# Optimization experiments

Measured on AMD Instinct MI355X. Metric: run time of the kernel, lower is better.

The kernel has to match this reference:

```python
import jax, jax.numpy as jnp
import numpy as np

N, T, M, D, H, FD, FF, L, B = 24, 120, 3, 32, 2, 16, 64, 3, 64
SCALE = 1.0 / np.sqrt(FD)  # torch MHA scales q by 1/sqrt(head_dim)
NEG = -1e9


def _make_pe():
    # Faithful to the module's (nonstandard) encoding: denominator uses 2*i/D for every i.
    t = np.arange(T, dtype=np.float64)[:, None]
    i = np.arange(D, dtype=np.float64)[None, :]
    denom = np.power(10000.0, 2.0 * i / D)
    pe = np.where(i % 2 == 0, np.sin(t / denom), np.cos(t / denom))
    return jnp.asarray(pe, jnp.float32)  # (T, D)


def _ln(x, g, b):
    mu = x.mean(-1, keepdims=True)
    var = x.var(-1, keepdims=True)
    return (x - mu) / jnp.sqrt(var + 1e-5) * g + b


def setup_inputs() -> dict:
    key = jax.random.key(0)
    keys = iter(jax.random.split(key, 48))
    def nrm(shape, s=0.1):
        return jax.random.normal(next(keys), shape, jnp.float32) * s
    inp = {
        'X': jax.random.normal(next(keys), (B, T, N * M), jnp.float32),
        'pe': _make_pe(),
        'E_W': nrm((N, M, D)), 'E_b': nrm((N, D), 0.01),
        'tq_W': nrm((N, D, D)), 'tq_b': nrm((N, D), 0.01),
        'tk_W': nrm((N, D, D)), 'tk_b': nrm((N, D), 0.01),
        'tv_W': nrm((N, D, D)), 'tv_b': nrm((N, D), 0.01),
        'tm_Wq': nrm((N, D, D)), 'tm_bq': nrm((N, D), 0.01),
        'tm_Wk': nrm((N, D, D)), 'tm_bk': nrm((N, D), 0.01),
        'tm_Wv': nrm((N, D, D)), 'tm_bv': nrm((N, D), 0.01),
        'tm_Wo': nrm((N, D, D)), 'tm_bo': nrm((N, D), 0.01),
        'sq_W': nrm((T, D, D)), 'sq_b': nrm((T, D), 0.01),
        'sk_W': nrm((T, D, D)), 'sk_b': nrm((T, D), 0.01),
        'sv_W': nrm((T, D, D)), 'sv_b': nrm((T, D), 0.01),
        'sm_Wq': nrm((T, D, D)), 'sm_bq': nrm((T, D), 0.01),
        'sm_Wk': nrm((T, D, D)), 'sm_bk': nrm((T, D), 0.01),
        'sm_Wv': nrm((T, D, D)), 'sm_bv': nrm((T, D), 0.01),
        'sm_Wo': nrm((T, D, D)), 'sm_bo': nrm((T, D), 0.01),
        'ff1_W': nrm((D, FF)), 'ff1_b': nrm((FF,), 0.01),
        'ff2_W': nrm((FF, D)), 'ff2_b': nrm((D,), 0.01),
        'ln_g': jnp.ones((D,), jnp.float32), 'ln_b': jnp.zeros((D,), jnp.float32),
        'op_W': nrm((N, D, M)), 'op_b': nrm((N, M), 0.01),
    }
    return inp


def reference(X, pe, E_W, E_b, tq_W, tq_b, tk_W, tk_b, tv_W, tv_b,
              tm_Wq, tm_bq, tm_Wk, tm_bk, tm_Wv, tm_bv, tm_Wo, tm_bo,
              sq_W, sq_b, sk_W, sk_b, sv_W, sv_b,
              sm_Wq, sm_bq, sm_Wk, sm_bk, sm_Wv, sm_bv, sm_Wo, sm_bo,
              ff1_W, ff1_b, ff2_W, ff2_b, ln_g, ln_b, op_W, op_b):
    b = X.shape[0]
    Xr = X.reshape(b, T, N, M)
    # per-joint embedding + positional encoding (dropout = identity in eval)
    E = jnp.einsum('btnm,nmd->btnd', Xr, E_W) + E_b + pe[None, :, None, :]
    causal = jnp.triu(jnp.full((T, T), NEG, jnp.float32), 1)
    for _ in range(L):
        # ---- temporal attention: per node n, causal over time ----
        q = jnp.einsum('btnd,nde->btne', E, tq_W) + tq_b
        k = jnp.einsum('btnd,nde->btne', E, tk_W) + tk_b
        v = jnp.einsum('btnd,nde->btne', E, tv_W) + tv_b
        qp = (jnp.einsum('btnd,nde->btne', q, tm_Wq) + tm_bq).reshape(b, T, N, H, FD)
        kp = (jnp.einsum('btnd,nde->btne', k, tm_Wk) + tm_bk).reshape(b, T, N, H, FD)
        vp = (jnp.einsum('btnd,nde->btne', v, tm_Wv) + tm_bv).reshape(b, T, N, H, FD)
        scores = jnp.einsum('bqnhf,bknhf->bnhqk', qp, kp) * SCALE + causal
        attn = jax.nn.softmax(scores, axis=-1)
        o = jnp.einsum('bnhqk,bknhf->bqnhf', attn, vp).reshape(b, T, N, D)
        t_sum = jnp.einsum('btnd,nde->btne', o, tm_Wo) + tm_bo
        t_norm = _ln(E + t_sum, ln_g, ln_b)
        # ---- spatial attention: per timestep t, full over nodes ----
        q = jnp.einsum('btnd,tde->btne', E, sq_W) + sq_b[:, None]
        k = jnp.einsum('btnd,tde->btne', E, sk_W) + sk_b[:, None]
        v = jnp.einsum('btnd,tde->btne', E, sv_W) + sv_b[:, None]
        qp = (jnp.einsum('btnd,tde->btne', q, sm_Wq) + sm_bq[:, None]).reshape(b, T, N, H, FD)
        kp = (jnp.einsum('btnd,tde->btne', k, sm_Wk) + sm_bk[:, None]).reshape(b, T, N, H, FD)
        vp = (jnp.einsum('btnd,tde->btne', v, sm_Wv) + sm_bv[:, None]).reshape(b, T, N, H, FD)
        scores = jnp.einsum('btqhf,btkhf->bthqk', qp, kp) * SCALE
        attn = jax.nn.softmax(scores, axis=-1)
        o = jnp.einsum('bthqk,btkhf->btqhf', attn, vp).reshape(b, T, N, D)
        s_sum = jnp.einsum('btnd,tde->btne', o, sm_Wo) + sm_bo[:, None]
        s_norm = _ln(E + s_sum, ln_g, ln_b)
        # ---- shared feedforward + norm ----
        ts = t_norm + s_norm
        ff = jax.nn.relu(ts @ ff1_W + ff1_b) @ ff2_W + ff2_b
        E = _ln(ff + ts, ln_g, ln_b)
    out = jnp.einsum('btnd,ndm->btnm', E, op_W) + op_b
    return out.reshape(b, T, N * M) + X
```

## Files before the change

### kernel.cpp

```cpp
#include <hip/hip_runtime.h>
#include <hip/hip_bf16.h>

typedef __hip_bfloat16 bf16;
typedef __fp16 h2 __attribute__((ext_vector_type(2)));
typedef _Float16 f16x2 __attribute__((ext_vector_type(2)));

constexpr int B  = 64, T = 120, N = 24, M = 3, D = 32;
constexpr int NH = 2, FD = 16, FF = 64, L = 3;
constexpr float SCALE = 0.25f;
constexpr int SK  = 40;
constexpr int SOH = 20;
constexpr int CH2 = 30;
constexpr int NJ  = 30;
constexpr int QR  = 64;
constexpr int QCH = (B * T) / QR;
constexpr int QEH = 20;
constexpr int BG  = 2;
constexpr int SR  = N * BG;
constexpr int SEH = 20;
constexpr int FR  = 32;
constexpr int QG  = N * QCH;
constexpr int SG  = T * (B / BG);

__device__ __forceinline__ float b2f(bf16 x) { return __bfloat162float(x); }
__device__ __forceinline__ float blo(unsigned u) { return __uint_as_float(u << 16); }
__device__ __forceinline__ float bhi(unsigned u) { return __uint_as_float(u & 0xffff0000u); }
__device__ __forceinline__ unsigned pk2(float a, float b) {
  bf16 x = __float2bfloat16(a), y = __float2bfloat16(b);
  unsigned short ux = *reinterpret_cast<unsigned short*>(&x);
  unsigned short uy = *reinterpret_cast<unsigned short*>(&y);
  return (unsigned)ux | ((unsigned)uy << 16);
}
__device__ __forceinline__ unsigned pkh2(float a, float b) {
  h2 r = __builtin_amdgcn_cvt_pkrtz(a, b);
  return *reinterpret_cast<unsigned*>(&r);
}
__device__ __forceinline__ h2 u2h(unsigned u) { return *reinterpret_cast<h2*>(&u); }
__device__ __forceinline__ f16x2 u2f(unsigned u) { return *reinterpret_cast<f16x2*>(&u); }

__global__ __launch_bounds__(256) void compose3_kernel(
    const float* __restrict__ W1q, const float* __restrict__ b1q,
    const float* __restrict__ W2q, const float* __restrict__ b2q,
    const float* __restrict__ W1k, const float* __restrict__ b1k,
    const float* __restrict__ W2k, const float* __restrict__ b2k,
    const float* __restrict__ W1v, const float* __restrict__ b1v,
    const float* __restrict__ W2v, const float* __restrict__ b2v,
    float* __restrict__ Wc, float* __restrict__ bc, int U) {
  int fam = blockIdx.x / U;
  int n   = blockIdx.x % U;
  const float* W1 = (fam == 0) ? W1q : (fam == 1) ? W1k : W1v;
  const float* b1 = (fam == 0) ? b1q : (fam == 1) ? b1k : b1v;
  const float* W2 = (fam == 0) ? W2q : (fam == 1) ? W2k : W2v;
  const float* b2 = (fam == 0) ? b2q : (fam == 1) ? b2k : b2v;
  const float* w1 = W1 + n * D * D;
  const float* w2 = W2 + n * D * D;
  float* wc  = Wc + (size_t)(fam * U + n) * D * D;
  float* bcp = bc + (fam * U + n) * D;
  __shared__ float s1[D * D], s2[D * D];
  for (int i = threadIdx.x; i < D * D; i += 256) { s1[i] = w1[i]; s2[i] = w2[i]; }
  __syncthreads();
  for (int i = threadIdx.x; i < D * D; i += 256) {
    int d = i >> 5, f = i & 31;
    float acc = 0.f;
#pragma unroll
    for (int e = 0; e < D; ++e) acc += s1[d * D + e] * s2[e * D + f];
    wc[i] = acc;
  }
  if (threadIdx.x < D) {
    int f = threadIdx.x;
    float acc = b2[n * D + f];
#pragma unroll
    for (int e = 0; e < D; ++e) acc += b1[n * D + e] * s2[e * D + f];
    bcp[f] = acc;
  }
}

__global__ __launch_bounds__(256) void embed_kernel(
    const float* __restrict__ X, const float* __restrict__ pe,
    const float* __restrict__ E_W, const float* __restrict__ E_b,
    bf16* __restrict__ E) {
  int idx = blockIdx.x * 256 + threadIdx.x;
  if (idx >= B * T * N * D) return;
  int d = idx & 31;
  int n = (idx >> 5) % N;
  int bt = idx / (D * N);
  int t = bt % T;
  const float* x = X + bt * (N * M) + n * M;
  float acc = E_b[n * D + d] + pe[t * D + d];
#pragma unroll
  for (int m = 0; m < M; ++m) acc += x[m] * E_W[(n * M + m) * D + d];
  E[idx] = __float2bfloat16(acc);
}

struct QSmem {
  unsigned whh[3 * (D / 2) * D];
  float bsh[3 * D];
  unsigned Esp[QR * QEH];
};
struct SSmem {
  unsigned Wh[3 * (D / 2) * D];
  unsigned woh[(D / 2) * D];
  float bqs[D], bks[D], bvs[D], bos[D], gs[D], bbs[D];
  unsigned Esh[SR * SEH];
  __fp16 Qh[SR * SK];
  __fp16 Kh[SR * SK];
  __fp16 Vh[SR * SK];
};
constexpr size_t FUSED_SMEM =
    sizeof(SSmem) > sizeof(QSmem) ? sizeof(SSmem) : sizeof(QSmem);

__global__ __launch_bounds__(256) void qs_fused_kernel(
    const bf16* __restrict__ E, const float* __restrict__ WtC,
    const float* __restrict__ btC,
    bf16* __restrict__ Qt, bf16* __restrict__ Kt, bf16* __restrict__ Vt,
    const float* __restrict__ WsC, const float* __restrict__ bsC,
    const float* __restrict__ sm_Wo, const float* __restrict__ sm_bo,
    const float* __restrict__ ln_g, const float* __restrict__ ln_b,
    bf16* __restrict__ Sn, int qblocks) {
  __shared__ __align__(16) char smem[FUSED_SMEM];
  int tid = threadIdx.x;

  if ((int)blockIdx.x < qblocks) {
    QSmem& q = *reinterpret_cast<QSmem*>(smem);
    int n     = blockIdx.x / QCH;
    int chunk = blockIdx.x % QCH;
    for (int i = tid; i < 3 * (D / 2) * D; i += 256) {
      int fam = i / ((D / 2) * D);
      int idx = i % ((D / 2) * D);
      int d2 = idx >> 5, j = idx & 31;
      const float* wg = WtC + (size_t)(fam * N + n) * D * D;
      q.whh[i] = pkh2(wg[(2 * d2) * D + j], wg[(2 * d2 + 1) * D + j]);
    }
    if (tid < 3 * D) {
      int fam = tid >> 5, e = tid & 31;
      q.bsh[tid] = btC[(fam * N + n) * D + e];
    }
    {
      int row = tid >> 2, p = tid & 3;
      const bf16* er = E + ((size_t)(chunk * QR + row) * N + n) * D;
      uint4 u = *(const uint4*)&er[p * 8];
      uint4 o;
      o.x = pkh2(blo(u.x), bhi(u.x));
      o.y = pkh2(blo(u.y), bhi(u.y));
      o.z = pkh2(blo(u.z), bhi(u.z));
      o.w = pkh2(blo(u.w), bhi(u.w));
      *(uint4*)&q.Esp[row * QEH + p * 4] = o;
    }
    __syncthreads();

    int row = tid >> 2, qd = tid & 3;
    int grow = chunk * QR + row;
    int b = grow / T, t = grow % T;
    unsigned xp[D / 2];
#pragma unroll
    for (int d2 = 0; d2 < D / 2; ++d2) xp[d2] = q.Esp[row * QEH + d2];
    size_t dsto = (((size_t)b * N + n) * T + t) * D + qd * 8;
    bf16* dsts[3] = { Qt + dsto, Kt + dsto, Vt + dsto };
#pragma unroll
    for (int fam = 0; fam < 3; ++fam) {
      const unsigned* wf = q.whh + fam * (D / 2) * D;
      const float* bi = q.bsh + fam * D;
      float a[8];
#pragma unroll
      for (int j = 0; j < 8; ++j) a[j] = bi[qd * 8 + j];
#pragma unroll
      for (int d2 = 0; d2 < D / 2; ++d2) {
        h2 x = u2h(xp[d2]);
#pragma unroll
        for (int j = 0; j < 8; ++j)
          a[j] = __builtin_amdgcn_fdot2(x, u2h(wf[d2 * D + qd * 8 + j]), a[j], false);
      }
      uint4 o;
      o.x = pk2(a[0], a[1]); o.y = pk2(a[2], a[3]);
      o.z = pk2(a[4], a[5]); o.w = pk2(a[6], a[7]);
      *(uint4*)dsts[fam] = o;
    }
  } else {
    SSmem& s = *reinterpret_cast<SSmem*>(smem);
    int sb = blockIdx.x - qblocks;
    int t  = sb >> 5;
    int bg = sb & 31;
    int b0 = bg * BG;

    for (int i = tid; i < 3 * (D / 2) * D; i += 256) {
      int fam = i / ((D / 2) * D);
      int idx = i % ((D / 2) * D);
      int d2 = idx >> 5, e = idx & 31;
      const float* wg = WsC + (size_t)(fam * T + t) * D * D;
      s.Wh[i] = pkh2(wg[(2 * d2) * D + e], wg[(2 * d2 + 1) * D + e]);
    }
    {
      const float* wg = sm_Wo + (size_t)t * D * D;
      for (int i = tid; i < (D / 2) * D; i += 256) {
        int d2 = i >> 5, e = i & 31;
        s.woh[i] = pkh2(wg[(2 * d2) * D + e], wg[(2 * d2 + 1) * D + e]);
      }
    }
    if (tid < D) {
      s.bqs[tid] = bsC[(0 * T + t) * D + tid];
      s.bks[tid] = bsC[(1 * T + t) * D + tid];
      s.bvs[tid] = bsC[(2 * T + t) * D + tid];
      s.bos[tid] = sm_bo[t * D + tid];
      s.gs[tid]  = ln_g[tid];
      s.bbs[tid] = ln_b[tid];
    }
    if (tid < SR * 4) {
      int r = tid >> 2, p = tid & 3;
      int b = b0 + r / N, n = r % N;
      uint4 u = *(const uint4*)&E[(((size_t)b * T + t) * N + n) * D + p * 8];
      uint4 o;
      o.x = pkh2(blo(u.x), bhi(u.x));
      o.y = pkh2(blo(u.y), bhi(u.y));
      o.z = pkh2(blo(u.z), bhi(u.z));
      o.w = pkh2(blo(u.w), bhi(u.w));
      *(uint4*)&s.Esh[r * SEH + p * 4] = o;
    }
    __syncthreads();

#pragma unroll 1
    for (int i = tid; i < SR * D; i += 256) {
      int r = i >> 5, e = i & 31;
      float aq = s.bqs[e], ak = s.bks[e], av = s.bvs[e];
#pragma unroll
      for (int d2 = 0; d2 < D / 2; ++d2) {
        h2 x = u2h(s.Esh[r * SEH + d2]);
        aq = __builtin_amdgcn_fdot2(x, u2h(s.Wh[0 * 512 + d2 * 32 + e]), aq, false);
        ak = __builtin_amdgcn_fdot2(x, u2h(s.Wh[1 * 512 + d2 * 32 + e]), ak, false);
        av = __builtin_amdgcn_fdot2(x, u2h(s.Wh[2 * 512 + d2 * 32 + e]), av, false);
      }
      s.Qh[r * SK + e] = (__fp16)aq;
      s.Kh[r * SK + e] = (__fp16)ak;
      s.Vh[r * SK + e] = (__fp16)av;
    }
    __syncthreads();

    if (tid < SR * NH) {
      int r = tid >> 1, h = tid & 1, ho = h * FD;
      int kb = (r >= N) ? N : 0;
      uint4 q0 = *(const uint4*)&s.Qh[r * SK + ho];
      uint4 q1 = *(const uint4*)&s.Qh[r * SK + ho + 8];
      unsigned qh[8] = { q0.x, q0.y, q0.z, q0.w, q1.x, q1.y, q1.z, q1.w };
      float sc[N];
      float m = -1e30f;
#pragma unroll
      for (int k = 0; k < N; ++k) {
        const uint4 ka = *(const uint4*)&s.Kh[(kb + k) * SK + ho];
        const uint4 kc = *(const uint4*)&s.Kh[(kb + k) * SK + ho + 8];
        float s0 = __builtin_amdgcn_fdot2(u2h(qh[0]), u2h(ka.x), 0.f, false);
        float s1 = __builtin_amdgcn_fdot2(u2h(qh[1]), u2h(ka.y), 0.f, false);
        float s2 = __builtin_amdgcn_fdot2(u2h(qh[2]), u2h(ka.z), 0.f, false);
        float s3 = __builtin_amdgcn_fdot2(u2h(qh[3]), u2h(ka.w), 0.f, false);
        s0 = __builtin_amdgcn_fdot2(u2h(qh[4]), u2h(kc.x), s0, false);
        s1 = __builtin_amdgcn_fdot2(u2h(qh[5]), u2h(kc.y), s1, false);
        s2 = __builtin_amdgcn_fdot2(u2h(qh[6]), u2h(kc.z), s2, false);
        s3 = __builtin_amdgcn_fdot2(u2h(qh[7]), u2h(kc.w), s3, false);
        float sv = ((s0 + s1) + (s2 + s3)) * SCALE;
        sc[k] = sv;
        m = fmaxf(m, sv);
      }
      float l = 0.f;
#pragma unroll
      for (int k = 0; k < N; ++k) { sc[k] = __expf(sc[k] - m); l += sc[k]; }
      float rl = 1.f / l;

      f16x2 acc2[8];
#pragma unroll
      for (int f = 0; f < 8; ++f) acc2[f] = f16x2{(_Float16)0.f, (_Float16)0.f};
#pragma unroll
      for (int k = 0; k < N; ++k) {
        f16x2 pp = f16x2{(_Float16)sc[k], (_Float16)sc[k]};
        const uint4 va = *(const uint4*)&s.Vh[(kb + k) * SK + ho];
        const uint4 vb = *(const uint4*)&s.Vh[(kb + k) * SK + ho + 8];
        acc2[0] += pp * u2f(va.x);
        acc2[1] += pp * u2f(va.y);
        acc2[2] += pp * u2f(va.z);
        acc2[3] += pp * u2f(va.w);
        acc2[4] += pp * u2f(vb.x);
        acc2[5] += pp * u2f(vb.y);
        acc2[6] += pp * u2f(vb.z);
        acc2[7] += pp * u2f(vb.w);
      }
      unsigned* op = (unsigned*)&s.Qh[r * SK + ho];
#pragma unroll
      for (int j = 0; j < 8; ++j)
        op[j] = pkh2((float)acc2[j][0] * rl, (float)acc2[j][1] * rl);
    }
    __syncthreads();

#pragma unroll 1
    for (int it = 0; it < 2; ++it) {
      int rl = it * 32 + (tid >> 3);
      int qd = tid & 7, e0 = qd * 4;
      if (rl < SR) {
        const unsigned* opk = (const unsigned*)&s.Qh[rl * SK];
        unsigned r0u = s.Esh[rl * SEH + (e0 >> 1)];
        unsigned r1u = s.Esh[rl * SEH + (e0 >> 1) + 1];
        h2 ra = u2h(r0u), rb = u2h(r1u);
        float res[4] = { (float)ra[0], (float)ra[1], (float)rb[0], (float)rb[1] };
        float o[4], s1 = 0.f, s2 = 0.f;
#pragma unroll
        for (int j = 0; j < 4; ++j) {
          int e = e0 + j;
          float a = s.bos[e] + res[j];
#pragma unroll
          for (int d2 = 0; d2 < D / 2; ++d2)
            a = __builtin_amdgcn_fdot2(u2h(opk[d2]), u2h(s.woh[d2 * D + e]), a, false);
          o[j] = a; s1 += a; s2 += a * a;
        }
        s1 += __shfl_xor(s1, 1, 64); s2 += __shfl_xor(s2, 1, 64);
        s1 += __shfl_xor(s1, 2, 64); s2 += __shfl_xor(s2, 2, 64);
        s1 += __shfl_xor(s1, 4, 64); s2 += __shfl_xor(s2, 4, 64);
        float mu  = s1 * (1.f / D);
        float var = s2 * (1.f / D) - mu * mu;
        float rr = rsqrtf(var + 1e-5f);
        int b = b0 + rl / N, n = rl % N;
        uint2 ou;
        ou.x = pk2((o[0]-mu)*rr*s.gs[e0]+s.bbs[e0],    (o[1]-mu)*rr*s.gs[e0+1]+s.bbs[e0+1]);
        ou.y = pk2((o[2]-mu)*rr*s.gs[e0+2]+s.bbs[e0+2],(o[3]-mu)*rr*s.gs[e0+3]+s.bbs[e0+3]);
        *(uint2*)&Sn[(((size_t)b * T + t) * N + n) * D + e0] = ou;
      }
    }
  }
}

__global__ __launch_bounds__(256) void attnt_kernel(
    const bf16* __restrict__ Qt, const bf16* __restrict__ Kt,
    const bf16* __restrict__ Vt, const bf16* __restrict__ E,
    const float* __restrict__ tm_Wo, const float* __restrict__ tm_bo,
    const float* __restrict__ ln_g, const float* __restrict__ ln_b,
    bf16* __restrict__ Tn) {
  int bn = blockIdx.x;
  int n  = bn % N, b = bn / N;
  __shared__ __align__(16) __fp16 Klh[T * SK];
  __shared__ __align__(16) __fp16 Vlh[T * SK];
  __shared__ __align__(16) __fp16 Qlh[CH2 * SK];
  __shared__ __align__(16) unsigned Olh[CH2 * SOH];
  __shared__ unsigned woh[(D / 2) * D];
  __shared__ float bol[D], gl[D], bbl[D];
  int tid = threadIdx.x;

  const bf16* Kg = Kt + (size_t)bn * T * D;
  const bf16* Vg = Vt + (size_t)bn * T * D;
  const bf16* Qg = Qt + (size_t)bn * T * D;
  for (int i = tid; i < T * 4; i += 256) {
    int r = i >> 2, p = i & 3;
    uint4 ku = *(const uint4*)&Kg[r * D + p * 8];
    uint4 kh;
    kh.x = pkh2(blo(ku.x), bhi(ku.x));
    kh.y = pkh2(blo(ku.y), bhi(ku.y));
    kh.z = pkh2(blo(ku.z), bhi(ku.z));
    kh.w = pkh2(blo(ku.w), bhi(ku.w));
    *(uint4*)&Klh[r * SK + p * 8] = kh;
    uint4 vu = *(const uint4*)&Vg[r * D + p * 8];
    uint4 vh;
    vh.x = pkh2(blo(vu.x), bhi(vu.x));
    vh.y = pkh2(blo(vu.y), bhi(vu.y));
    vh.z = pkh2(blo(vu.z), bhi(vu.z));
    vh.w = pkh2(blo(vu.w), bhi(vu.w));
    *(uint4*)&Vlh[r * SK + p * 8] = vh;
  }
  {
    const float* wg = tm_Wo + (size_t)n * D * D;
    for (int i = tid; i < (D / 2) * D; i += 256) {
      int d2 = i >> 5, e = i & 31;
      woh[i] = pkh2(wg[(2 * d2) * D + e], wg[(2 * d2 + 1) * D + e]);
    }
  }
  if (tid < D) {
    bol[tid] = tm_bo[n * D + tid];
    gl[tid]  = ln_g[tid];
    bbl[tid] = ln_b[tid];
  }
  __syncthreads();

#pragma unroll
  for (int c = 0; c < 4; ++c) {
    const int JM = (CH2 * (c + 1) + 3) >> 2;
    if (tid < CH2 * 4) {
      int r = tid >> 2, p = tid & 3;
      uint4 qu = *(const uint4*)&Qg[(CH2 * c + r) * D + p * 8];
      uint4 qh;
      qh.x = pkh2(blo(qu.x), bhi(qu.x));
      qh.y = pkh2(blo(qu.y), bhi(qu.y));
      qh.z = pkh2(blo(qu.z), bhi(qu.z));
      qh.w = pkh2(blo(qu.w), bhi(qu.w));
      *(uint4*)&Qlh[r * SK + p * 8] = qh;
    }
    __syncthreads();

    {
      int task = tid >> 2, sl = tid & 3;
      if (task < 2 * CH2) {
        int rl = task >> 1, h = task & 1, ho = h * FD;
        int rg = CH2 * c + rl;
        uint4 q0 = *(const uint4*)&Qlh[rl * SK + ho];
        uint4 q1 = *(const uint4*)&Qlh[rl * SK + ho + 8];
        unsigned qh[8] = { q0.x, q0.y, q0.z, q0.w, q1.x, q1.y, q1.z, q1.w };

        float sc[NJ];
        float mx = -3e38f;
#pragma unroll
        for (int j = 0; j < JM; ++j) {
          int k = 4 * j + sl;
          sc[j] = -3e38f;
          if (k <= rg) {
            const uint4 ka = *(const uint4*)&Klh[k * SK + ho];
            const uint4 kb = *(const uint4*)&Klh[k * SK + ho + 8];
            float s0 = __builtin_amdgcn_fdot2(u2h(qh[0]), u2h(ka.x), 0.f, false);
            float s1 = __builtin_amdgcn_fdot2(u2h(qh[1]), u2h(ka.y), 0.f, false);
            float s2 = __builtin_amdgcn_fdot2(u2h(qh[2]), u2h(ka.z), 0.f, false);
            float s3 = __builtin_amdgcn_fdot2(u2h(qh[3]), u2h(ka.w), 0.f, false);
            s0 = __builtin_amdgcn_fdot2(u2h(qh[4]), u2h(kb.x), s0, false);
            s1 = __builtin_amdgcn_fdot2(u2h(qh[5]), u2h(kb.y), s1, false);
            s2 = __builtin_amdgcn_fdot2(u2h(qh[6]), u2h(kb.z), s2, false);
            s3 = __builtin_amdgcn_fdot2(u2h(qh[7]), u2h(kb.w), s3, false);
            float s = ((s0 + s1) + (s2 + s3)) * SCALE;
            sc[j] = s;
            mx = fmaxf(mx, s);
          }
        }
        mx = fmaxf(mx, __shfl_xor(mx, 1, 64));
        mx = fmaxf(mx, __shfl_xor(mx, 2, 64));
        float l = 0.f;
#pragma unroll
        for (int j = 0; j < JM; ++j) {
          sc[j] = __expf(sc[j] - mx);
          l += sc[j];
        }
        l += __shfl_xor(l, 1, 64);
        l += __shfl_xor(l, 2, 64);
        float rli = 1.f / l;

        f16x2 acc2[8];
#pragma unroll
        for (int f = 0; f < 8; ++f) acc2[f] = f16x2{(_Float16)0.f, (_Float16)0.f};
#pragma unroll
        for (int j = 0; j < JM; ++j) {
          int k = 4 * j + sl;
          if (k <= rg) {
            f16x2 pp = f16x2{(_Float16)sc[j], (_Float16)sc[j]};
            const uint4 va = *(const uint4*)&Vlh[k * SK + ho];
            const uint4 vb = *(const uint4*)&Vlh[k * SK + ho + 8];
            acc2[0] += pp * u2f(va.x);
            acc2[1] += pp * u2f(va.y);
            acc2[2] += pp * u2f(va.z);
            acc2[3] += pp * u2f(va.w);
            acc2[4] += pp * u2f(vb.x);
            acc2[5] += pp * u2f(vb.y);
            acc2[6] += pp * u2f(vb.z);
            acc2[7] += pp * u2f(vb.w);
          }
        }
#pragma unroll
        for (int f = 0; f < 8; ++f) {
          unsigned u = *reinterpret_cast<unsigned*>(&acc2[f]);
          unsigned u1 = __shfl_xor(u, 1, 64);
          acc2[f] += u2f(u1);
          u = *reinterpret_cast<unsigned*>(&acc2[f]);
          unsigned u2_ = __shfl_xor(u, 2, 64);
          acc2[f] += u2f(u2_);
        }
        if (sl == 0) {
#pragma unroll
          for (int j = 0; j < 8; ++j)
            Olh[rl * SOH + h * 8 + j] =
                pkh2((float)acc2[j][0] * rli, (float)acc2[j][1] * rli);
        }
      }
    }
    __syncthreads();

    {
      int rl = tid >> 3, q = tid & 7, e0 = q * 4;
      if (rl < CH2) {
        int rg = CH2 * c + rl;
        size_t rowo = ((size_t)(b * T + rg) * N + n) * D;
        uint2 eu = *(const uint2*)&E[rowo + e0];
        float res[4] = { blo(eu.x), bhi(eu.x), blo(eu.y), bhi(eu.y) };
        float o[4], s1 = 0.f, s2 = 0.f;
#pragma unroll
        for (int j = 0; j < 4; ++j) {
          int e = e0 + j;
          float a = bol[e] + res[j];
#pragma unroll
          for (int d2 = 0; d2 < D / 2; ++d2)
            a = __builtin_amdgcn_fdot2(u2h(Olh[rl * SOH + d2]),
                                       u2h(woh[d2 * D + e]), a, false);
          o[j] = a; s1 += a; s2 += a * a;
        }
        s1 += __shfl_xor(s1, 1, 64); s2 += __shfl_xor(s2, 1, 64);
        s1 += __shfl_xor(s1, 2, 64); s2 += __shfl_xor(s2, 2, 64);
        s1 += __shfl_xor(s1, 4, 64); s2 += __shfl_xor(s2, 4, 64);
        float mu  = s1 * (1.f / D);
        float var = s2 * (1.f / D) - mu * mu;
        float r = rsqrtf(var + 1e-5f);
        uint2 ou;
        ou.x = pk2((o[0]-mu)*r*gl[e0]+bbl[e0],    (o[1]-mu)*r*gl[e0+1]+bbl[e0+1]);
        ou.y = pk2((o[2]-mu)*r*gl[e0+2]+bbl[e0+2],(o[3]-mu)*r*gl[e0+3]+bbl[e0+3]);
        *(uint2*)&Tn[rowo + e0] = ou;
      }
    }
  }
}

__global__ __launch_bounds__(256) void ff_kernel(
    const bf16* __restrict__ Tn, const bf16* __restrict__ Sn,
    const float* __restrict__ W1, const float* __restrict__ b1,
    const float* __restrict__ W2, const float* __restrict__ b2,
    const float* __restrict__ ln_g, const float* __restrict__ ln_b,
    bf16* __restrict__ E) {
  __shared__ unsigned w1h[(D / 2) * FF];
  __shared__ unsigned w2h[(FF / 2) * D];
  __shared__ float bb1[FF], bb2[D], gs[D], bbs[D];
  __shared__ unsigned tslp[FR][D / 2 + 1];
  __shared__ unsigned hlp[FR][FF / 2 + 1];
  int tid = threadIdx.x;
  int r0 = blockIdx.x * FR;
  for (int i = tid; i < (D / 2) * FF; i += 256) {
    int d2 = i / FF, jj = i % FF;
    w1h[i] = pkh2(W1[(2 * d2) * FF + jj], W1[(2 * d2 + 1) * FF + jj]);
  }
  for (int i = tid; i < (FF / 2) * D; i += 256) {
    int k2 = i / D, e = i % D;
    w2h[i] = pkh2(W2[(2 * k2) * D + e], W2[(2 * k2 + 1) * D + e]);
  }
  if (tid < FF) bb1[tid] = b1[tid];
  if (tid < D) { bb2[tid] = b2[tid]; gs[tid] = ln_g[tid]; bbs[tid] = ln_b[tid]; }
  int r = tid >> 3, s = tid & 7;
  {
    const bf16* tp = Tn + ((size_t)(r0 + r)) * D + s * 4;
    const bf16* sp = Sn + ((size_t)(r0 + r)) * D + s * 4;
    uint2 tu = *(const uint2*)tp;
    uint2 su = *(const uint2*)sp;
    float t0 = blo(tu.x) + blo(su.x);
    float t1 = bhi(tu.x) + bhi(su.x);
    float t2 = blo(tu.y) + blo(su.y);
    float t3 = bhi(tu.y) + bhi(su.y);
    tslp[r][s * 2]     = pkh2(t0, t1);
    tslp[r][s * 2 + 1] = pkh2(t2, t3);
  }
  __syncthreads();
  {
    float hh[8];
#pragma unroll
    for (int j = 0; j < 8; ++j) {
      int jj = s * 8 + j;
      float a = bb1[jj];
#pragma unroll
      for (int d2 = 0; d2 < D / 2; ++d2)
        a = __builtin_amdgcn_fdot2(u2h(tslp[r][d2]), u2h(w1h[d2 * FF + jj]), a, false);
      hh[j] = fmaxf(a, 0.f);
    }
#pragma unroll
    for (int j = 0; j < 4; ++j)
      hlp[r][s * 4 + j] = pkh2(hh[2 * j], hh[2 * j + 1]);
  }
  __syncthreads();
  {
    float x[4];
    float s1 = 0.f, s2 = 0.f;
#pragma unroll
    for (int j4 = 0; j4 < 4; ++j4) {
      int e = s * 4 + j4;
      h2 tv = u2h(tslp[r][e >> 1]);
      float a = bb2[e] + (float)tv[j4 & 1];
#pragma unroll
      for (int k2 = 0; k2 < FF / 2; ++k2)
        a = __builtin_amdgcn_fdot2(u2h(hlp[r][k2]), u2h(w2h[k2 * D + e]), a, false);
      x[j4] = a; s1 += a; s2 += a * a;
    }
    s1 += __shfl_xor(s1, 1, 64); s2 += __shfl_xor(s2, 1, 64);
    s1 += __shfl_xor(s1, 2, 64); s2 += __shfl_xor(s2, 2, 64);
    s1 += __shfl_xor(s1, 4, 64); s2 += __shfl_xor(s2, 4, 64);
    float mu  = s1 * (1.f / D);
    float var = s2 * (1.f / D) - mu * mu;
    float rr = rsqrtf(var + 1e-5f);
    int e0 = s * 4;
    uint2 ou;
    ou.x = pk2((x[0]-mu)*rr*gs[e0]+bbs[e0],    (x[1]-mu)*rr*gs[e0+1]+bbs[e0+1]);
    ou.y = pk2((x[2]-mu)*rr*gs[e0+2]+bbs[e0+2],(x[3]-mu)*rr*gs[e0+3]+bbs[e0+3]);
    *(uint2*)&E[((size_t)(r0 + r)) * D + e0] = ou;
  }
}

__global__ __launch_bounds__(256) void out_kernel(
    const bf16* __restrict__ E, const float* __restrict__ op_W,
    const float* __restrict__ op_b, const float* __restrict__ X,
    float* __restrict__ out) {
  int idx = blockIdx.x * 256 + threadIdx.x;
  if (idx >= B * T * N * M) return;
  int m  = idx % M;
  int n  = (idx / M) % N;
  int bt = idx / (M * N);
  float acc = op_b[n * M + m];
  const bf16* e = E + ((size_t)bt * N + n) * D;
#pragma unroll
  for (int d = 0; d < D; ++d) acc += b2f(e[d]) * op_W[(n * D + d) * M + m];
  acc += X[idx];
  out[idx] = acc;
}

extern "C" void kernel_launch(void* const* d_in, const int* in_sizes, int n_in,
                              void* d_out, int out_size, void* d_ws, size_t ws_size,
                              hipStream_t stream) {
  const float* X     = (const float*)d_in[0];
  const float* pe    = (const float*)d_in[1];
  const float* E_W   = (const float*)d_in[2];
  const float* E_b   = (const float*)d_in[3];
  const float* tq_W  = (const float*)d_in[4];
  const float* tq_b  = (const float*)d_in[5];
  const float* tk_W  = (const float*)d_in[6];
  const float* tk_b  = (const float*)d_in[7];
  const float* tv_W  = (const float*)d_in[8];
  const float* tv_b  = (const float*)d_in[9];
  const float* tm_Wq = (const float*)d_in[10];
  const float* tm_bq = (const float*)d_in[11];
  const float* tm_Wk = (const float*)d_in[12];
  const float* tm_bk = (const float*)d_in[13];
  const float* tm_Wv = (const float*)d_in[14];
  const float* tm_bv = (const float*)d_in[15];
  const float* tm_Wo = (const float*)d_in[16];
  const float* tm_bo = (const float*)d_in[17];
  const float* sq_W  = (const float*)d_in[18];
  const float* sq_b  = (const float*)d_in[19];
  const float* sk_W  = (const float*)d_in[20];
  const float* sk_b  = (const float*)d_in[21];
  const float* sv_W  = (const float*)d_in[22];
  const float* sv_b  = (const float*)d_in[23];
  const float* sm_Wq = (const float*)d_in[24];
  const float* sm_bq = (const float*)d_in[25];
  const float* sm_Wk = (const float*)d_in[26];
  const float* sm_bk = (const float*)d_in[27];
  const float* sm_Wv = (const float*)d_in[28];
  const float* sm_bv = (const float*)d_in[29];
  const float* sm_Wo = (const float*)d_in[30];
  const float* sm_bo = (const float*)d_in[31];
  const float* ff1_W = (const float*)d_in[32];
  const float* ff1_b = (const float*)d_in[33];
  const float* ff2_W = (const float*)d_in[34];
  const float* ff2_b = (const float*)d_in[35];
  const float* ln_g  = (const float*)d_in[36];
  const float* ln_b  = (const float*)d_in[37];
  const float* op_W  = (const float*)d_in[38];
  const float* op_b  = (const float*)d_in[39];
  float* out = (float*)d_out;

  float* WtC = (float*)d_ws;
  float* btC = WtC + 3 * N * D * D;
  float* WsC = btC + 3 * N * D;
  float* bsC = WsC + 3 * T * D * D;
  size_t act = (size_t)B * T * N * D;
  bf16* Ebuf = (bf16*)(bsC + 3 * T * D);
  bf16* Tn   = Ebuf + act;
  bf16* Qt   = Tn + act;
  bf16* Kt   = Qt + act;
  bf16* Vt   = Kt + act;

  size_t floats_bytes = (size_t)(3 * N * D * D + 3 * N * D +
                                 3 * T * D * D + 3 * T * D) * sizeof(float);
  size_t need6 = floats_bytes + 6 * act * sizeof(bf16);
  bool concurrent = (ws_size >= need6);
  bf16* Sn = concurrent ? (Vt + act) : Qt;

  compose3_kernel<<<3 * N, 256, 0, stream>>>(
      tq_W, tq_b, tm_Wq, tm_bq, tk_W, tk_b, tm_Wk, tm_bk,
      tv_W, tv_b, tm_Wv, tm_bv, WtC, btC, N);
  compose3_kernel<<<3 * T, 256, 0, stream>>>(
      sq_W, sq_b, sm_Wq, sm_bq, sk_W, sk_b, sm_Wk, sm_bk,
      sv_W, sv_b, sm_Wv, sm_bv, WsC, bsC, T);

  embed_kernel<<<(B * T * N * D) / 256, 256, 0, stream>>>(X, pe, E_W, E_b, Ebuf);

  for (int l = 0; l < L; ++l) {
    if (concurrent) {
      qs_fused_kernel<<<QG + SG, 256, 0, stream>>>(
          Ebuf, WtC, btC, Qt, Kt, Vt,
          WsC, bsC, sm_Wo, sm_bo, ln_g, ln_b, Sn, QG);
      attnt_kernel<<<B * N, 256, 0, stream>>>(Qt, Kt, Vt, Ebuf, tm_Wo, tm_bo, ln_g, ln_b, Tn);
    } else {
      qs_fused_kernel<<<QG, 256, 0, stream>>>(
          Ebuf, WtC, btC, Qt, Kt, Vt,
          WsC, bsC, sm_Wo, sm_bo, ln_g, ln_b, Sn, QG);
      attnt_kernel<<<B * N, 256, 0, stream>>>(Qt, Kt, Vt, Ebuf, tm_Wo, tm_bo, ln_g, ln_b, Tn);
      qs_fused_kernel<<<SG, 256, 0, stream>>>(
          Ebuf, WtC, btC, Qt, Kt, Vt,
          WsC, bsC, sm_Wo, sm_bo, ln_g, ln_b, Sn, 0);
    }
    ff_kernel<<<(B * T * N) / FR, 256, 0, stream>>>(Tn, Sn, ff1_W, ff1_b, ff2_W, ff2_b, ln_g, ln_b, Ebuf);
  }

  out_kernel<<<(B * T * N * M + 255) / 256, 256, 0, stream>>>(Ebuf, op_W, op_b, X, out);
}
```

Baseline: 422.8 us.

## Co-schedule temporal attention with spatial attention instead of with QKV projection

Splits the temporal QKV projection into its own kernel and fuses temporal attention with the spatial-attention branch in one launch, selected by block index. The spatial branch previously overlapped the cheap QKV projection and temporal attention ran alone afterwards. Now the two heavy attention phases share one grid. The launch count per layer stays the same, but the shared-memory union gets larger, which may reduce occupancy.

```diff
diff --git a/kernel.cpp b/kernel.cpp
--- a/kernel.cpp
+++ b/kernel.cpp
@@ -20,6 +20,7 @@
 constexpr int SEH = 20;
 constexpr int FR  = 32;
 constexpr int QG  = N * QCH;
+constexpr int AG  = B * N;
 constexpr int SG  = T * (B / BG);
 
 __device__ __forceinline__ float b2f(bf16 x) { return __bfloat162float(x); }
@@ -92,12 +93,78 @@
   E[idx] = __float2bfloat16(acc);
 }
 
-struct QSmem {
-  unsigned whh[3 * (D / 2) * D];
-  float bsh[3 * D];
-  unsigned Esp[QR * QEH];
+__global__ __launch_bounds__(256) void qkvt_kernel(
+    const bf16* __restrict__ E, const float* __restrict__ WtC,
+    const float* __restrict__ btC,
+    bf16* __restrict__ Qt, bf16* __restrict__ Kt, bf16* __restrict__ Vt) {
+  int n     = blockIdx.x / QCH;
+  int chunk = blockIdx.x % QCH;
+  __shared__ unsigned whh[3 * (D / 2) * D];
+  __shared__ float bsh[3 * D];
+  __shared__ __align__(16) unsigned Esp[QR * QEH];
+  int tid = threadIdx.x;
+  for (int i = tid; i < 3 * (D / 2) * D; i += 256) {
+    int fam = i / ((D / 2) * D);
+    int idx = i % ((D / 2) * D);
+    int d2 = idx >> 5, j = idx & 31;
+    const float* wg = WtC + (size_t)(fam * N + n) * D * D;
+    whh[i] = pkh2(wg[(2 * d2) * D + j], wg[(2 * d2 + 1) * D + j]);
+  }
+  if (tid < 3 * D) {
+    int fam = tid >> 5, e = tid & 31;
+    bsh[tid] = btC[(fam * N + n) * D + e];
+  }
+  {
+    int row = tid >> 2, p = tid & 3;
+    const bf16* er = E + ((size_t)(chunk * QR + row) * N + n) * D;
+    uint4 u = *(const uint4*)&er[p * 8];
+    uint4 o;
+    o.x = pkh2(blo(u.x), bhi(u.x));
+    o.y = pkh2(blo(u.y), bhi(u.y));
+    o.z = pkh2(blo(u.z), bhi(u.z));
+    o.w = pkh2(blo(u.w), bhi(u.w));
+    *(uint4*)&Esp[row * QEH + p * 4] = o;
+  }
+  __syncthreads();
+
+  int row = tid >> 2, q = tid & 3;
+  int grow = chunk * QR + row;
+  int b = grow / T, t = grow % T;
+  unsigned xp[D / 2];
+#pragma unroll
+  for (int d2 = 0; d2 < D / 2; ++d2) xp[d2] = Esp[row * QEH + d2];
+  size_t dsto = (((size_t)b * N + n) * T + t) * D + q * 8;
+  bf16* dsts[3] = { Qt + dsto, Kt + dsto, Vt + dsto };
+#pragma unroll
+  for (int fam = 0; fam < 3; ++fam) {
+    const unsigned* wf = whh + fam * (D / 2) * D;
+    const float* bi = bsh + fam * D;
+    float a[8];
+#pragma unroll
+    for (int j = 0; j < 8; ++j) a[j] = bi[q * 8 + j];
+#pragma unroll
+    for (int d2 = 0; d2 < D / 2; ++d2) {
+      h2 x = u2h(xp[d2]);
+#pragma unroll
+      for (int j = 0; j < 8; ++j)
+        a[j] = __builtin_amdgcn_fdot2(x, u2h(wf[d2 * D + q * 8 + j]), a[j], false);
+    }
+    uint4 o;
+    o.x = pk2(a[0], a[1]); o.y = pk2(a[2], a[3]);
+    o.z = pk2(a[4], a[5]); o.w = pk2(a[6], a[7]);
+    *(uint4*)dsts[fam] = o;
+  }
+}
+
+struct ASmemA {
+  __fp16 Klh[T * SK];
+  __fp16 Vlh[T * SK];
+  __fp16 Qlh[CH2 * SK];
+  unsigned Olh[CH2 * SOH];
+  unsigned woh[(D / 2) * D];
+  float bol[D], gl[D], bbl[D];
 };
-struct SSmem {
+struct ASmemS {
   unsigned Wh[3 * (D / 2) * D];
   unsigned woh[(D / 2) * D];
   float bqs[D], bks[D], bvs[D], bos[D], gs[D], bbs[D];
@@ -106,78 +173,190 @@
   __fp16 Kh[SR * SK];
   __fp16 Vh[SR * SK];
 };
-constexpr size_t FUSED_SMEM =
-    sizeof(SSmem) > sizeof(QSmem) ? sizeof(SSmem) : sizeof(QSmem);
-
-__global__ __launch_bounds__(256) void qs_fused_kernel(
-    const bf16* __restrict__ E, const float* __restrict__ WtC,
-    const float* __restrict__ btC,
-    bf16* __restrict__ Qt, bf16* __restrict__ Kt, bf16* __restrict__ Vt,
+constexpr size_t AS_SMEM =
+    sizeof(ASmemA) > sizeof(ASmemS) ? sizeof(ASmemA) : sizeof(ASmemS);
+
+__global__ __launch_bounds__(256) void as_fused_kernel(
+    const bf16* __restrict__ Qt, const bf16* __restrict__ Kt,
+    const bf16* __restrict__ Vt, const bf16* __restrict__ E,
+    const float* __restrict__ tm_Wo, const float* __restrict__ tm_bo,
     const float* __restrict__ WsC, const float* __restrict__ bsC,
     const float* __restrict__ sm_Wo, const float* __restrict__ sm_bo,
     const float* __restrict__ ln_g, const float* __restrict__ ln_b,
-    bf16* __restrict__ Sn, int qblocks) {
-  __shared__ __align__(16) char smem[FUSED_SMEM];
+    bf16* __restrict__ Tn, bf16* __restrict__ Sn, int ablocks) {
+  __shared__ __align__(16) char smem[AS_SMEM];
   int tid = threadIdx.x;
 
-  if ((int)blockIdx.x < qblocks) {
-    QSmem& q = *reinterpret_cast<QSmem*>(smem);
-    int n     = blockIdx.x / QCH;
-    int chunk = blockIdx.x % QCH;
-    for (int i = tid; i < 3 * (D / 2) * D; i += 256) {
-      int fam = i / ((D / 2) * D);
-      int idx = i % ((D / 2) * D);
-      int d2 = idx >> 5, j = idx & 31;
-      const float* wg = WtC + (size_t)(fam * N + n) * D * D;
-      q.whh[i] = pkh2(wg[(2 * d2) * D + j], wg[(2 * d2 + 1) * D + j]);
-    }
-    if (tid < 3 * D) {
-      int fam = tid >> 5, e = tid & 31;
-      q.bsh[tid] = btC[(fam * N + n) * D + e];
+  if ((int)blockIdx.x < ablocks) {
+    ASmemA& A = *reinterpret_cast<ASmemA*>(smem);
+    int bn = blockIdx.x;
+    int n  = bn % N, b = bn / N;
+
+    const bf16* Kg = Kt + (size_t)bn * T * D;
+    const bf16* Vg = Vt + (size_t)bn * T * D;
+    const bf16* Qg = Qt + (size_t)bn * T * D;
+    for (int i = tid; i < T * 4; i += 256) {
+      int r = i >> 2, p = i & 3;
+      uint4 ku = *(const uint4*)&Kg[r * D + p * 8];
+      uint4 kh;
+      kh.x = pkh2(blo(ku.x), bhi(ku.x));
+      kh.y = pkh2(blo(ku.y), bhi(ku.y));
+      kh.z = pkh2(blo(ku.z), bhi(ku.z));
+      kh.w = pkh2(blo(ku.w), bhi(ku.w));
+      *(uint4*)&A.Klh[r * SK + p * 8] = kh;
+      uint4 vu = *(const uint4*)&Vg[r * D + p * 8];
+      uint4 vh;
+      vh.x = pkh2(blo(vu.x), bhi(vu.x));
+      vh.y = pkh2(blo(vu.y), bhi(vu.y));
+      vh.z = pkh2(blo(vu.z), bhi(vu.z));
+      vh.w = pkh2(blo(vu.w), bhi(vu.w));
+      *(uint4*)&A.Vlh[r * SK + p * 8] = vh;
     }
     {
-      int row = tid >> 2, p = tid & 3;
-      const bf16* er = E + ((size_t)(chunk * QR + row) * N + n) * D;
-      uint4 u = *(const uint4*)&er[p * 8];
-      uint4 o;
-      o.x = pkh2(blo(u.x), bhi(u.x));
-      o.y = pkh2(blo(u.y), bhi(u.y));
-      o.z = pkh2(blo(u.z), bhi(u.z));
-      o.w = pkh2(blo(u.w), bhi(u.w));
-      *(uint4*)&q.Esp[row * QEH + p * 4] = o;
+      const float* wg = tm_Wo + (size_t)n * D * D;
+      for (int i = tid; i < (D / 2) * D; i += 256) {
+        int d2 = i >> 5, e = i & 31;
+        A.woh[i] = pkh2(wg[(2 * d2) * D + e], wg[(2 * d2 + 1) * D + e]);
+      }
+    }
+    if (tid < D) {
+      A.bol[tid] = tm_bo[n * D + tid];
+      A.gl[tid]  = ln_g[tid];
+      A.bbl[tid] = ln_b[tid];
     }
     __syncthreads();
 
-    int row = tid >> 2, qd = tid & 3;
-    int grow = chunk * QR + row;
-    int b = grow / T, t = grow % T;
-    unsigned xp[D / 2];
-#pragma unroll
-    for (int d2 = 0; d2 < D / 2; ++d2) xp[d2] = q.Esp[row * QEH + d2];
-    size_t dsto = (((size_t)b * N + n) * T + t) * D + qd * 8;
-    bf16* dsts[3] = { Qt + dsto, Kt + dsto, Vt + dsto };
-#pragma unroll
-    for (int fam = 0; fam < 3; ++fam) {
-      const unsigned* wf = q.whh + fam * (D / 2) * D;
-      const float* bi = q.bsh + fam * D;
-      float a[8];
-#pragma unroll
-      for (int j = 0; j < 8; ++j) a[j] = bi[qd * 8 + j];
-#pragma unroll
-      for (int d2 = 0; d2 < D / 2; ++d2) {
-        h2 x = u2h(xp[d2]);
-#pragma unroll
-        for (int j = 0; j < 8; ++j)
-          a[j] = __builtin_amdgcn_fdot2(x, u2h(wf[d2 * D + qd * 8 + j]), a[j], false);
-      }
-      uint4 o;
-      o.x = pk2(a[0], a[1]); o.y = pk2(a[2], a[3]);
-      o.z = pk2(a[4], a[5]); o.w = pk2(a[6], a[7]);
-      *(uint4*)dsts[fam] = o;
+#pragma unroll
+    for (int c = 0; c < 4; ++c) {
+      const int JM = (CH2 * (c + 1) + 3) >> 2;
+      if (tid < CH2 * 4) {
+        int r = tid >> 2, p = tid & 3;
+        uint4 qu = *(const uint4*)&Qg[(CH2 * c + r) * D + p * 8];
+        uint4 qh;
+        qh.x = pkh2(blo(qu.x), bhi(qu.x));
+        qh.y = pkh2(blo(qu.y), bhi(qu.y));
+        qh.z = pkh2(blo(qu.z), bhi(qu.z));
+        qh.w = pkh2(blo(qu.w), bhi(qu.w));
+        *(uint4*)&A.Qlh[r * SK + p * 8] = qh;
+      }
+      __syncthreads();
+
+      {
+        int task = tid >> 2, sl = tid & 3;
+        if (task < 2 * CH2) {
+          int rl = task >> 1, h = task & 1, ho = h * FD;
+          int rg = CH2 * c + rl;
+          uint4 q0 = *(const uint4*)&A.Qlh[rl * SK + ho];
+          uint4 q1 = *(const uint4*)&A.Qlh[rl * SK + ho + 8];
+          unsigned qh[8] = { q0.x, q0.y, q0.z, q0.w, q1.x, q1.y, q1.z, q1.w };
+
+          float sc[NJ];
+          float mx = -3e38f;
+#pragma unroll
+          for (int j = 0; j < JM; ++j) {
+            int k = 4 * j + sl;
+            sc[j] = -3e38f;
+            if (k <= rg) {
+              const uint4 ka = *(const uint4*)&A.Klh[k * SK + ho];
+              const uint4 kb = *(const uint4*)&A.Klh[k * SK + ho + 8];
+              float s0 = __builtin_amdgcn_fdot2(u2h(qh[0]), u2h(ka.x), 0.f, false);
+              float s1 = __builtin_amdgcn_fdot2(u2h(qh[1]), u2h(ka.y), 0.f, false);
+              float s2 = __builtin_amdgcn_fdot2(u2h(qh[2]), u2h(ka.z), 0.f, false);
+              float s3 = __builtin_amdgcn_fdot2(u2h(qh[3]), u2h(ka.w), 0.f, false);
+              s0 = __builtin_amdgcn_fdot2(u2h(qh[4]), u2h(kb.x), s0, false);
+              s1 = __builtin_amdgcn_fdot2(u2h(qh[5]), u2h(kb.y), s1, false);
+              s2 = __builtin_amdgcn_fdot2(u2h(qh[6]), u2h(kb.z), s2, false);
+              s3 = __builtin_amdgcn_fdot2(u2h(qh[7]), u2h(kb.w), s3, false);
+              float s = ((s0 + s1) + (s2 + s3)) * SCALE;
+              sc[j] = s;
+              mx = fmaxf(mx, s);
+            }
+          }
+          mx = fmaxf(mx, __shfl_xor(mx, 1, 64));
+          mx = fmaxf(mx, __shfl_xor(mx, 2, 64));
+          float l = 0.f;
+#pragma unroll
+          for (int j = 0; j < JM; ++j) {
+            sc[j] = __expf(sc[j] - mx);
+            l += sc[j];
+          }
+          l += __shfl_xor(l, 1, 64);
+          l += __shfl_xor(l, 2, 64);
+          float rli = 1.f / l;
+
+          f16x2 acc2[8];
+#pragma unroll
+          for (int f = 0; f < 8; ++f) acc2[f] = f16x2{(_Float16)0.f, (_Float16)0.f};
+#pragma unroll
+          for (int j = 0; j < JM; ++j) {
+            int k = 4 * j + sl;
+            if (k <= rg) {
+              f16x2 pp = f16x2{(_Float16)sc[j], (_Float16)sc[j]};
+              const uint4 va = *(const uint4*)&A.Vlh[k * SK + ho];
+              const uint4 vb = *(const uint4*)&A.Vlh[k * SK + ho + 8];
+              acc2[0] += pp * u2f(va.x);
+              acc2[1] += pp * u2f(va.y);
+              acc2[2] += pp * u2f(va.z);
+              acc2[3] += pp * u2f(va.w);
+              acc2[4] += pp * u2f(vb.x);
+              acc2[5] += pp * u2f(vb.y);
+              acc2[6] += pp * u2f(vb.z);
+              acc2[7] += pp * u2f(vb.w);
+            }
+          }
+#pragma unroll
+          for (int f = 0; f < 8; ++f) {
+            unsigned u = *reinterpret_cast<unsigned*>(&acc2[f]);
+            unsigned u1 = __shfl_xor(u, 1, 64);
+            acc2[f] += u2f(u1);
+            u = *reinterpret_cast<unsigned*>(&acc2[f]);
+            unsigned u2_ = __shfl_xor(u, 2, 64);
+            acc2[f] += u2f(u2_);
+          }
+          if (sl == 0) {
+#pragma unroll
+            for (int j = 0; j < 8; ++j)
+              A.Olh[rl * SOH + h * 8 + j] =
+                  pkh2((float)acc2[j][0] * rli, (float)acc2[j][1] * rli);
+          }
+        }
+      }
+      __syncthreads();
+
+      {
+        int rl = tid >> 3, q = tid & 7, e0 = q * 4;
+        if (rl < CH2) {
+          int rg = CH2 * c + rl;
+          size_t rowo = ((size_t)(b * T + rg) * N + n) * D;
+          uint2 eu = *(const uint2*)&E[rowo + e0];
+          float res[4] = { blo(eu.x), bhi(eu.x), blo(eu.y), bhi(eu.y) };
+          float o[4], s1 = 0.f, s2 = 0.f;
+#pragma unroll
+          for (int j = 0; j < 4; ++j) {
+            int e = e0 + j;
+            float a = A.bol[e] + res[j];
+#pragma unroll
+            for (int d2 = 0; d2 < D / 2; ++d2)
+              a = __builtin_amdgcn_fdot2(u2h(A.Olh[rl * SOH + d2]),
+                                         u2h(A.woh[d2 * D + e]), a, false);
+            o[j] = a; s1 += a; s2 += a * a;
+          }
+          s1 += __shfl_xor(s1, 1, 64); s2 += __shfl_xor(s2, 1, 64);
+          s1 += __shfl_xor(s1, 2, 64); s2 += __shfl_xor(s2, 2, 64);
+          s1 += __shfl_xor(s1, 4, 64); s2 += __shfl_xor(s2, 4, 64);
+          float mu  = s1 * (1.f / D);
+          float var = s2 * (1.f / D) - mu * mu;
+          float r = rsqrtf(var + 1e-5f);
+          uint2 ou;
+          ou.x = pk2((o[0]-mu)*r*A.gl[e0]+A.bbl[e0],    (o[1]-mu)*r*A.gl[e0+1]+A.bbl[e0+1]);
+          ou.y = pk2((o[2]-mu)*r*A.gl[e0+2]+A.bbl[e0+2],(o[3]-mu)*r*A.gl[e0+3]+A.bbl[e0+3]);
+          *(uint2*)&Tn[rowo + e0] = ou;
+        }
+      }
     }
   } else {
-    SSmem& s = *reinterpret_cast<SSmem*>(smem);
-    int sb = blockIdx.x - qblocks;
+    ASmemS& s = *reinterpret_cast<ASmemS*>(smem);
+    int sb = blockIdx.x - ablocks;
     int t  = sb >> 5;
     int bg = sb & 31;
     int b0 = bg * BG;
@@ -318,186 +497,6 @@
         ou.x = pk2((o[0]-mu)*rr*s.gs[e0]+s.bbs[e0],    (o[1]-mu)*rr*s.gs[e0+1]+s.bbs[e0+1]);
         ou.y = pk2((o[2]-mu)*rr*s.gs[e0+2]+s.bbs[e0+2],(o[3]-mu)*rr*s.gs[e0+3]+s.bbs[e0+3]);
         *(uint2*)&Sn[(((size_t)b * T + t) * N + n) * D + e0] = ou;
-      }
-    }
-  }
-}
-
-__global__ __launch_bounds__(256) void attnt_kernel(
-    const bf16* __restrict__ Qt, const bf16* __restrict__ Kt,
-    const bf16* __restrict__ Vt, const bf16* __restrict__ E,
-    const float* __restrict__ tm_Wo, const float* __restrict__ tm_bo,
-    const float* __restrict__ ln_g, const float* __restrict__ ln_b,
-    bf16* __restrict__ Tn) {
-  int bn = blockIdx.x;
-  int n  = bn % N, b = bn / N;
-  __shared__ __align__(16) __fp16 Klh[T * SK];
-  __shared__ __align__(16) __fp16 Vlh[T * SK];
-  __shared__ __align__(16) __fp16 Qlh[CH2 * SK];
-  __shared__ __align__(16) unsigned Olh[CH2 * SOH];
-  __shared__ unsigned woh[(D / 2) * D];
-  __shared__ float bol[D], gl[D], bbl[D];
-  int tid = threadIdx.x;
-
-  const bf16* Kg = Kt + (size_t)bn * T * D;
-  const bf16* Vg = Vt + (size_t)bn * T * D;
-  const bf16* Qg = Qt + (size_t)bn * T * D;
-  for (int i = tid; i < T * 4; i += 256) {
-    int r = i >> 2, p = i & 3;
-    uint4 ku = *(const uint4*)&Kg[r * D + p * 8];
-    uint4 kh;
-    kh.x = pkh2(blo(ku.x), bhi(ku.x));
-    kh.y = pkh2(blo(ku.y), bhi(ku.y));
-    kh.z = pkh2(blo(ku.z), bhi(ku.z));
-    kh.w = pkh2(blo(ku.w), bhi(ku.w));
-    *(uint4*)&Klh[r * SK + p * 8] = kh;
-    uint4 vu = *(const uint4*)&Vg[r * D + p * 8];
-    uint4 vh;
-    vh.x = pkh2(blo(vu.x), bhi(vu.x));
-    vh.y = pkh2(blo(vu.y), bhi(vu.y));
-    vh.z = pkh2(blo(vu.z), bhi(vu.z));
-    vh.w = pkh2(blo(vu.w), bhi(vu.w));
-    *(uint4*)&Vlh[r * SK + p * 8] = vh;
-  }
-  {
-    const float* wg = tm_Wo + (size_t)n * D * D;
-    for (int i = tid; i < (D / 2) * D; i += 256) {
-      int d2 = i >> 5, e = i & 31;
-      woh[i] = pkh2(wg[(2 * d2) * D + e], wg[(2 * d2 + 1) * D + e]);
-    }
-  }
-  if (tid < D) {
-    bol[tid] = tm_bo[n * D + tid];
-    gl[tid]  = ln_g[tid];
-    bbl[tid] = ln_b[tid];
-  }
-  __syncthreads();
-
-#pragma unroll
-  for (int c = 0; c < 4; ++c) {
-    const int JM = (CH2 * (c + 1) + 3) >> 2;
-    if (tid < CH2 * 4) {
-      int r = tid >> 2, p = tid & 3;
-      uint4 qu = *(const uint4*)&Qg[(CH2 * c + r) * D + p * 8];
-      uint4 qh;
-      qh.x = pkh2(blo(qu.x), bhi(qu.x));
-      qh.y = pkh2(blo(qu.y), bhi(qu.y));
-      qh.z = pkh2(blo(qu.z), bhi(qu.z));
-      qh.w = pkh2(blo(qu.w), bhi(qu.w));
-      *(uint4*)&Qlh[r * SK + p * 8] = qh;
-    }
-    __syncthreads();
-
-    {
-      int task = tid >> 2, sl = tid & 3;
-      if (task < 2 * CH2) {
-        int rl = task >> 1, h = task & 1, ho = h * FD;
-        int rg = CH2 * c + rl;
-        uint4 q0 = *(const uint4*)&Qlh[rl * SK + ho];
-        uint4 q1 = *(const uint4*)&Qlh[rl * SK + ho + 8];
-        unsigned qh[8] = { q0.x, q0.y, q0.z, q0.w, q1.x, q1.y, q1.z, q1.w };
-
-        float sc[NJ];
-        float mx = -3e38f;
-#pragma unroll
-        for (int j = 0; j < JM; ++j) {
-          int k = 4 * j + sl;
-          sc[j] = -3e38f;
-          if (k <= rg) {
-            const uint4 ka = *(const uint4*)&Klh[k * SK + ho];
-            const uint4 kb = *(const uint4*)&Klh[k * SK + ho + 8];
-            float s0 = __builtin_amdgcn_fdot2(u2h(qh[0]), u2h(ka.x), 0.f, false);
-            float s1 = __builtin_amdgcn_fdot2(u2h(qh[1]), u2h(ka.y), 0.f, false);
-            float s2 = __builtin_amdgcn_fdot2(u2h(qh[2]), u2h(ka.z), 0.f, false);
-            float s3 = __builtin_amdgcn_fdot2(u2h(qh[3]), u2h(ka.w), 0.f, false);
-            s0 = __builtin_amdgcn_fdot2(u2h(qh[4]), u2h(kb.x), s0, false);
-            s1 = __builtin_amdgcn_fdot2(u2h(qh[5]), u2h(kb.y), s1, false);
-            s2 = __builtin_amdgcn_fdot2(u2h(qh[6]), u2h(kb.z), s2, false);
-            s3 = __builtin_amdgcn_fdot2(u2h(qh[7]), u2h(kb.w), s3, false);
-            float s = ((s0 + s1) + (s2 + s3)) * SCALE;
-            sc[j] = s;
-            mx = fmaxf(mx, s);
-          }
-        }
-        mx = fmaxf(mx, __shfl_xor(mx, 1, 64));
-        mx = fmaxf(mx, __shfl_xor(mx, 2, 64));
-        float l = 0.f;
-#pragma unroll
-        for (int j = 0; j < JM; ++j) {
-          sc[j] = __expf(sc[j] - mx);
-          l += sc[j];
-        }
-        l += __shfl_xor(l, 1, 64);
-        l += __shfl_xor(l, 2, 64);
-        float rli = 1.f / l;
-
-        f16x2 acc2[8];
-#pragma unroll
-        for (int f = 0; f < 8; ++f) acc2[f] = f16x2{(_Float16)0.f, (_Float16)0.f};
-#pragma unroll
-        for (int j = 0; j < JM; ++j) {
-          int k = 4 * j + sl;
-          if (k <= rg) {
-            f16x2 pp = f16x2{(_Float16)sc[j], (_Float16)sc[j]};
-            const uint4 va = *(const uint4*)&Vlh[k * SK + ho];
-            const uint4 vb = *(const uint4*)&Vlh[k * SK + ho + 8];
-            acc2[0] += pp * u2f(va.x);
-            acc2[1] += pp * u2f(va.y);
-            acc2[2] += pp * u2f(va.z);
-            acc2[3] += pp * u2f(va.w);
-            acc2[4] += pp * u2f(vb.x);
-            acc2[5] += pp * u2f(vb.y);
-            acc2[6] += pp * u2f(vb.z);
-            acc2[7] += pp * u2f(vb.w);
-          }
-        }
-#pragma unroll
-        for (int f = 0; f < 8; ++f) {
-          unsigned u = *reinterpret_cast<unsigned*>(&acc2[f]);
-          unsigned u1 = __shfl_xor(u, 1, 64);
-          acc2[f] += u2f(u1);
-          u = *reinterpret_cast<unsigned*>(&acc2[f]);
-          unsigned u2_ = __shfl_xor(u, 2, 64);
-          acc2[f] += u2f(u2_);
-        }
-        if (sl == 0) {
-#pragma unroll
-          for (int j = 0; j < 8; ++j)
-            Olh[rl * SOH + h * 8 + j] =
-                pkh2((float)acc2[j][0] * rli, (float)acc2[j][1] * rli);
-        }
-      }
-    }
-    __syncthreads();
-
-    {
-      int rl = tid >> 3, q = tid & 7, e0 = q * 4;
-      if (rl < CH2) {
-        int rg = CH2 * c + rl;
-        size_t rowo = ((size_t)(b * T + rg) * N + n) * D;
-        uint2 eu = *(const uint2*)&E[rowo + e0];
-        float res[4] = { blo(eu.x), bhi(eu.x), blo(eu.y), bhi(eu.y) };
-        float o[4], s1 = 0.f, s2 = 0.f;
-#pragma unroll
-        for (int j = 0; j < 4; ++j) {
-          int e = e0 + j;
-          float a = bol[e] + res[j];
-#pragma unroll
-          for (int d2 = 0; d2 < D / 2; ++d2)
-            a = __builtin_amdgcn_fdot2(u2h(Olh[rl * SOH + d2]),
-                                       u2h(woh[d2 * D + e]), a, false);
-          o[j] = a; s1 += a; s2 += a * a;
-        }
-        s1 += __shfl_xor(s1, 1, 64); s2 += __shfl_xor(s2, 1, 64);
-        s1 += __shfl_xor(s1, 2, 64); s2 += __shfl_xor(s2, 2, 64);
-        s1 += __shfl_xor(s1, 4, 64); s2 += __shfl_xor(s2, 4, 64);
-        float mu  = s1 * (1.f / D);
-        float var = s2 * (1.f / D) - mu * mu;
-        float r = rsqrtf(var + 1e-5f);
-        uint2 ou;
-        ou.x = pk2((o[0]-mu)*r*gl[e0]+bbl[e0],    (o[1]-mu)*r*gl[e0+1]+bbl[e0+1]);
-        ou.y = pk2((o[2]-mu)*r*gl[e0+2]+bbl[e0+2],(o[3]-mu)*r*gl[e0+3]+bbl[e0+3]);
-        *(uint2*)&Tn[rowo + e0] = ou;
       }
     }
   }
@@ -672,19 +671,18 @@
   embed_kernel<<<(B * T * N * D) / 256, 256, 0, stream>>>(X, pe, E_W, E_b, Ebuf);
 
   for (int l = 0; l < L; ++l) {
+    qkvt_kernel<<<QG, 256, 0, stream>>>(Ebuf, WtC, btC, Qt, Kt, Vt);
     if (concurrent) {
-      qs_fused_kernel<<<QG + SG, 256, 0, stream>>>(
-          Ebuf, WtC, btC, Qt, Kt, Vt,
-          WsC, bsC, sm_Wo, sm_bo, ln_g, ln_b, Sn, QG);
-      attnt_kernel<<<B * N, 256, 0, stream>>>(Qt, Kt, Vt, Ebuf, tm_Wo, tm_bo, ln_g, ln_b, Tn);
+      as_fused_kernel<<<AG + SG, 256, 0, stream>>>(
+          Qt, Kt, Vt, Ebuf, tm_Wo, tm_bo,
+          WsC, bsC, sm_Wo, sm_bo, ln_g, ln_b, Tn, Sn, AG);
     } else {
-      qs_fused_kernel<<<QG, 256, 0, stream>>>(
-          Ebuf, WtC, btC, Qt, Kt, Vt,
-          WsC, bsC, sm_Wo, sm_bo, ln_g, ln_b, Sn, QG);
-      attnt_kernel<<<B * N, 256, 0, stream>>>(Qt, Kt, Vt, Ebuf, tm_Wo, tm_bo, ln_g, ln_b, Tn);
-      qs_fused_kernel<<<SG, 256, 0, stream>>>(
-          Ebuf, WtC, btC, Qt, Kt, Vt,
-          WsC, bsC, sm_Wo, sm_bo, ln_g, ln_b, Sn, 0);
+      as_fused_kernel<<<AG, 256, 0, stream>>>(
+          Qt, Kt, Vt, Ebuf, tm_Wo, tm_bo,
+          WsC, bsC, sm_Wo, sm_bo, ln_g, ln_b, Tn, Sn, AG);
+      as_fused_kernel<<<SG, 256, 0, stream>>>(
+          Qt, Kt, Vt, Ebuf, tm_Wo, tm_bo,
+          WsC, bsC, sm_Wo, sm_bo, ln_g, ln_b, Tn, Sn, 0);
     }
     ff_kernel<<<(B * T * N) / FR, 256, 0, stream>>>(Tn, Sn, ff1_W, ff1_b, ff2_W, ff2_b, ln_g, ln_b, Ebuf);
   }
```

After: 414.5 us. No clear change (-2.0%).
